# Kernel optimization log

Measured on AMD Instinct MI355X. Metric: run time of the kernel, lower is better.

The kernel has to match this reference:

```python
import jax, jax.numpy as jnp
import numpy as np

RES, K, H = 8192, 48, 128

def _layer_norm(x, g, b, eps=1e-5):
    mu = jnp.mean(x, axis=-1, keepdims=True)
    var = jnp.var(x, axis=-1, keepdims=True)
    return (x - mu) * jax.lax.rsqrt(var + eps) * g + b

def _gelu(x):
    return jax.nn.gelu(x, approximate=False)  # torch default exact GELU

def setup_inputs() -> dict:
    key = jax.random.key(0)
    ks = jax.random.split(key, 16)
    s = 0.05
    inp = {
        "node_h": jax.random.normal(ks[0], (RES, H), jnp.float32),
        "edge_h": jax.random.normal(ks[1], (RES, K, H), jnp.float32),
        "edge_idx": jax.random.randint(ks[2], (RES, K), 0, RES, jnp.int32),
        "seq_emb": jax.random.normal(ks[3], (RES, H), jnp.float32),
        "ar_mask": jax.random.uniform(ks[4], (RES, K), jnp.float32),
        # msg_mlp: Linear(4h,h) -> GELU -> Linear(h,h) -> GELU -> Linear(h,h)
        "mW1": jax.random.normal(ks[5], (4 * H, H), jnp.float32) * s,
        "mb1": jnp.zeros((H,), jnp.float32),
        "mW2": jax.random.normal(ks[6], (H, H), jnp.float32) * s,
        "mb2": jnp.zeros((H,), jnp.float32),
        "mW3": jax.random.normal(ks[7], (H, H), jnp.float32) * s,
        "mb3": jnp.zeros((H,), jnp.float32),
        # ff_node: Linear(h,4h) -> GELU -> Linear(4h,h)
        "fW1": jax.random.normal(ks[8], (H, 4 * H), jnp.float32) * s,
        "fb1": jnp.zeros((4 * H,), jnp.float32),
        "fW2": jax.random.normal(ks[9], (4 * H, H), jnp.float32) * s,
        "fb2": jnp.zeros((H,), jnp.float32),
        "g1": jnp.ones((H,), jnp.float32), "b1": jnp.zeros((H,), jnp.float32),
        "g2": jnp.ones((H,), jnp.float32), "b2": jnp.zeros((H,), jnp.float32),
    }
    return inp

def reference(node_h, edge_h, edge_idx, seq_emb, ar_mask,
              mW1, mb1, mW2, mb2, mW3, mb3,
              fW1, fb1, fW2, fb2, g1, b1, g2, b2):
    seq_j = seq_emb[edge_idx] * ar_mask[..., None]           # [res,k,h]
    e_dec = jnp.concatenate([edge_h, seq_j], axis=-1)        # [res,k,2h]
    h_j = node_h[edge_idx]                                   # [res,k,h]
    h_i = jnp.broadcast_to(node_h[:, None, :], (node_h.shape[0], edge_idx.shape[1], node_h.shape[1]))
    x = jnp.concatenate([h_i, h_j, e_dec], axis=-1)          # [res,k,4h]
    msg = _gelu(x @ mW1 + mb1)
    msg = _gelu(msg @ mW2 + mb2)
    msg = msg @ mW3 + mb3                                    # [res,k,h]
    agg = jnp.sum(msg, axis=1)                               # [res,h]
    h = _layer_norm(node_h + agg, g1, b1)
    ff = _gelu(h @ fW1 + fb1) @ fW2 + fb2
    h = _layer_norm(h + ff, g2, b2)
    return h
```

## Files before the change

### kernel.cpp

```cpp
#include <hip/hip_runtime.h>

#define KNB 48

typedef float  floatx4 __attribute__((ext_vector_type(4)));
typedef __bf16 bf16x8  __attribute__((ext_vector_type(8)));
typedef unsigned short ushort8  __attribute__((ext_vector_type(8)));
typedef unsigned short ushort4v __attribute__((ext_vector_type(4)));

__device__ __forceinline__ float bf2f(unsigned short b) {
  union { unsigned int u; float f; } v; v.u = ((unsigned int)b) << 16; return v.f;
}
__device__ __forceinline__ unsigned short f2bf(float f) {
  __bf16 h = (__bf16)f;
  union { __bf16 h; unsigned short u; } v; v.h = h; return v.u;
}
__device__ __forceinline__ float gelu_f(float x) {
  float u = x * (0.7978845608f + 0.0356774081f * x * x);
  float t = __builtin_amdgcn_exp2f(u * -2.8853900818f);
  return x * __builtin_amdgcn_rcpf(1.0f + t);
}

__global__ __launch_bounds__(256) void k0_transpose(
    const float* mW1, const float* mW2, const float* mW3,
    const float* fW1, const float* fW2,
    unsigned short* MT1, unsigned short* WT2, unsigned short* WT3,
    unsigned short* FWT1, unsigned short* FWT2) {
  __shared__ unsigned short tile[32][33];
  int b = blockIdx.x;
  const float* src; unsigned short* dst; int Kd, Nd, t;
  if (b < 64)       { src = mW1; dst = MT1;  Kd = 512; Nd = 128; t = b; }
  else if (b < 80)  { src = mW2; dst = WT2;  Kd = 128; Nd = 128; t = b - 64; }
  else if (b < 96)  { src = mW3; dst = WT3;  Kd = 128; Nd = 128; t = b - 80; }
  else if (b < 160) { src = fW1; dst = FWT1; Kd = 128; Nd = 512; t = b - 96; }
  else              { src = fW2; dst = FWT2; Kd = 512; Nd = 128; t = b - 160; }
  int tN = Nd >> 5;
  int tk = t / tN, tn = t % tN;
  int tx = threadIdx.x & 31, ty = threadIdx.x >> 5;
  for (int r = 0; r < 4; ++r) {
    int row = ty + r * 8;
    tile[row][tx] = f2bf(src[(size_t)(tk * 32 + row) * Nd + tn * 32 + tx]);
  }
  __syncthreads();
  for (int r = 0; r < 4; ++r) {
    int row = ty + r * 8;
    dst[(size_t)(tn * 32 + row) * Kd + tk * 32 + tx] = tile[tx][row];
  }
}

__global__ __launch_bounds__(256) void k1_nodepre(
    const float* node_h, const float* seq_emb,
    const unsigned short* MT1, const float* mb1,
    float* Apr, unsigned short* BS) {
  __shared__ __align__(16) unsigned short sX[2][32 * 128];
  int r0 = blockIdx.x * 32;
  int tid = threadIdx.x, lane = tid & 63, w = tid >> 6;
  int l15 = lane & 15, l16 = lane >> 4;

  for (int mset = 0; mset < 2; ++mset) {
    const float* src = mset ? (seq_emb + (size_t)r0 * 128) : (node_h + (size_t)r0 * 128);
    for (int k = 0; k < 4; ++k) {
      int f = tid + 256 * k;
      floatx4 v = ((const floatx4*)src)[f];
      int row = f >> 5, hc = f & 31, c = hc >> 1, half = hc & 1;
      ushort4v o;
      o[0] = f2bf(v[0]); o[1] = f2bf(v[1]); o[2] = f2bf(v[2]); o[3] = f2bf(v[3]);
      *(ushort4v*)((char*)&sX[mset][0] + row * 256 + ((c ^ (row & 7)) << 4) + half * 8) = o;
    }
  }
  __syncthreads();

  for (int q = 0; q < 6; ++q) {
    int job = w + 4 * q;
    int kind = job >> 3;
    int nt = job & 7;
    int colOff = (kind == 0) ? 0 : (kind == 1) ? 128 : 384;
    const unsigned short* X = sX[kind == 2 ? 1 : 0];
    bf16x8 wf[4];
    for (int kk = 0; kk < 4; ++kk)
      wf[kk] = *(const bf16x8*)(MT1 + (size_t)(nt * 16 + l15) * 512 + colOff + kk * 32 + l16 * 8);
    for (int mt = 0; mt < 2; ++mt) {
      floatx4 acc = {0.f, 0.f, 0.f, 0.f};
      for (int kk = 0; kk < 4; ++kk) {
        int row = mt * 16 + l15;
        int off = (kk * 64 + l16 * 16) ^ ((row & 7) << 4);
        bf16x8 a = *(const bf16x8*)((const char*)X + row * 256 + off);
        acc = __builtin_amdgcn_mfma_f32_16x16x32_bf16(a, wf[kk], acc, 0, 0, 0);
      }
      int col = nt * 16 + l15;
      for (int r = 0; r < 4; ++r) {
        int row = r0 + mt * 16 + l16 * 4 + r;
        if (kind == 0)      Apr[(size_t)row * 128 + col] = acc[r] + mb1[col];
        else if (kind == 1) BS[(size_t)row * 256 + col] = f2bf(acc[r]);
        else                BS[(size_t)row * 256 + 128 + col] = f2bf(acc[r]);
      }
    }
  }
}

__global__ __launch_bounds__(256) void k2_edge(
    const float* edge_h, const int* edge_idx, const float* ar_mask,
    const unsigned short* MT1, const unsigned short* WT2, const unsigned short* WT3,
    const float* mb2, const float* mb3,
    const float* Apr, const unsigned short* BS,
    float* agg) {
  __shared__ __align__(16) unsigned short sE[96 * 128];
  __shared__ __align__(16) unsigned short sT[96 * 128];
  __shared__ int   sJ[96];
  __shared__ float sM[96];
  int i0 = blockIdx.x * 2;
  int tid = threadIdx.x, lane = tid & 63, w = tid >> 6;
  int l15 = lane & 15, l16 = lane >> 4;
  int rb = (l16 & 1) * 4;

  if (tid < 96) {
    sJ[tid] = edge_idx[(size_t)i0 * KNB + tid];
    sM[tid] = ar_mask[(size_t)i0 * KNB + tid];
  }
  const float* eb = edge_h + (size_t)i0 * KNB * 128;
  for (int k = 0; k < 12; ++k) {
    int f = tid + 256 * k;
    floatx4 v = ((const floatx4*)eb)[f];
    int row = f >> 5, hc = f & 31, c = hc >> 1, half = hc & 1;
    ushort4v o;
    o[0] = f2bf(v[0]); o[1] = f2bf(v[1]); o[2] = f2bf(v[2]); o[3] = f2bf(v[3]);
    *(ushort4v*)((char*)sE + row * 256 + ((c ^ (row & 7)) << 4) + half * 8) = o;
  }
  __syncthreads();

  for (int u = tid; u < 96 * 16; u += 256) {
    int e = u >> 4, c8 = u & 15;
    int j = sJ[e]; float m = sM[e];
    int i = i0 + (e >= 48 ? 1 : 0);
    const floatx4* ap = (const floatx4*)(Apr + (size_t)i * 128 + c8 * 8);
    floatx4 a0 = ap[0], a1 = ap[1];
    ushort8 vb = *(const ushort8*)(BS + (size_t)j * 256 + c8 * 8);
    ushort8 vs = *(const ushort8*)(BS + (size_t)j * 256 + 128 + c8 * 8);
    ushort8 res;
#pragma unroll
    for (int x = 0; x < 4; ++x)
      res[x] = f2bf(a0[x] + bf2f(vb[x]) + m * bf2f(vs[x]));
#pragma unroll
    for (int x = 0; x < 4; ++x)
      res[4 + x] = f2bf(a1[x] + bf2f(vb[4 + x]) + m * bf2f(vs[4 + x]));
    *(ushort8*)((char*)sT + e * 256 + ((c8 ^ (e & 7)) * 16)) = res;
  }
  __syncthreads();

  {
    bf16x8 wf[2][4];
    for (int n = 0; n < 2; ++n)
      for (int kk = 0; kk < 4; ++kk)
        wf[n][kk] = *(const bf16x8*)(MT1 + (size_t)((2 * w + n) * 16 + l15) * 512 + 256 + kk * 32 + l16 * 8);
    int cp0 = ((((2 * w) * 16 + l15) >> 3) << 4) | ((l15 & 7) << 1);
    int cp1 = ((((2 * w + 1) * 16 + l15) >> 3) << 4) | ((l15 & 7) << 1);
    for (int mt = 0; mt < 6; ++mt) {
      floatx4 acc0 = {0.f,0.f,0.f,0.f}, acc1 = {0.f,0.f,0.f,0.f};
      for (int kk = 0; kk < 4; ++kk) {
        int row = mt * 16 + l15;
        int off = (kk * 64 + l16 * 16) ^ ((row & 7) << 4);
        bf16x8 a = *(const bf16x8*)((const char*)sE + row * 256 + off);
        acc0 = __builtin_amdgcn_mfma_f32_16x16x32_bf16(a, wf[0][kk], acc0, 0, 0, 0);
        acc1 = __builtin_amdgcn_mfma_f32_16x16x32_bf16(a, wf[1][kk], acc1, 0, 0, 0);
      }
      char* base = (char*)sT + (mt * 16 + l16 * 4) * 256;
#pragma unroll
      for (int r = 0; r < 4; ++r) {
        int sw = (rb + r) << 4;
        char* p0 = base + r * 256 + (cp0 ^ sw);
        char* p1 = base + r * 256 + (cp1 ^ sw);
        float g0 = bf2f(*(unsigned short*)p0);
        float g1v = bf2f(*(unsigned short*)p1);
        *(unsigned short*)p0 = f2bf(gelu_f(acc0[r] + g0));
        *(unsigned short*)p1 = f2bf(gelu_f(acc1[r] + g1v));
      }
    }
  }
  __syncthreads();

  {
    bf16x8 wf[2][4];
    for (int n = 0; n < 2; ++n)
      for (int kk = 0; kk < 4; ++kk)
        wf[n][kk] = *(const bf16x8*)(WT2 + (size_t)((2 * w + n) * 16 + l15) * 128 + kk * 32 + l16 * 8);
    int cp0 = ((((2 * w) * 16 + l15) >> 3) << 4) | ((l15 & 7) << 1);
    int cp1 = ((((2 * w + 1) * 16 + l15) >> 3) << 4) | ((l15 & 7) << 1);
    float bb0 = mb2[(2 * w) * 16 + l15];
    float bb1 = mb2[(2 * w + 1) * 16 + l15];
    for (int mt = 0; mt < 6; ++mt) {
      floatx4 acc0 = {0.f,0.f,0.f,0.f}, acc1 = {0.f,0.f,0.f,0.f};
      for (int kk = 0; kk < 4; ++kk) {
        int row = mt * 16 + l15;
        int off = (kk * 64 + l16 * 16) ^ ((row & 7) << 4);
        bf16x8 a = *(const bf16x8*)((const char*)sT + row * 256 + off);
        acc0 = __builtin_amdgcn_mfma_f32_16x16x32_bf16(a, wf[0][kk], acc0, 0, 0, 0);
        acc1 = __builtin_amdgcn_mfma_f32_16x16x32_bf16(a, wf[1][kk], acc1, 0, 0, 0);
      }
      char* base = (char*)sE + (mt * 16 + l16 * 4) * 256;
#pragma unroll
      for (int r = 0; r < 4; ++r) {
        int sw = (rb + r) << 4;
        *(unsigned short*)(base + r * 256 + (cp0 ^ sw)) = f2bf(gelu_f(acc0[r] + bb0));
        *(unsigned short*)(base + r * 256 + (cp1 ^ sw)) = f2bf(gelu_f(acc1[r] + bb1));
      }
    }
  }
  __syncthreads();

  {
    bf16x8 wf[2][4];
    for (int n = 0; n < 2; ++n)
      for (int kk = 0; kk < 4; ++kk)
        wf[n][kk] = *(const bf16x8*)(WT3 + (size_t)((2 * w + n) * 16 + l15) * 128 + kk * 32 + l16 * 8);
    for (int half = 0; half < 2; ++half) {
      float agga[2][4] = {{0.f,0.f,0.f,0.f},{0.f,0.f,0.f,0.f}};
      for (int mt3 = 0; mt3 < 3; ++mt3) {
        int mt = half * 3 + mt3;
        floatx4 acc0 = {0.f,0.f,0.f,0.f}, acc1 = {0.f,0.f,0.f,0.f};
        for (int kk = 0; kk < 4; ++kk) {
          int row = mt * 16 + l15;
          int off = (kk * 64 + l16 * 16) ^ ((row & 7) << 4);
          bf16x8 a = *(const bf16x8*)((const char*)sE + row * 256 + off);
          acc0 = __builtin_amdgcn_mfma_f32_16x16x32_bf16(a, wf[0][kk], acc0, 0, 0, 0);
          acc1 = __builtin_amdgcn_mfma_f32_16x16x32_bf16(a, wf[1][kk], acc1, 0, 0, 0);
        }
#pragma unroll
        for (int r = 0; r < 4; ++r) { agga[0][r] += acc0[r]; agga[1][r] += acc1[r]; }
      }
      for (int n = 0; n < 2; ++n) {
        float s = agga[n][0] + agga[n][1] + agga[n][2] + agga[n][3];
        s += __shfl_xor(s, 16);
        s += __shfl_xor(s, 32);
        if (lane < 16) {
          int col = (2 * w + n) * 16 + lane;
          agg[(size_t)(i0 + half) * 128 + col] = s + 48.0f * mb3[col];
        }
      }
    }
  }
}

__global__ __launch_bounds__(256) void k3_ff(
    const float* node_h, const float* agg,
    const unsigned short* FWT1, const unsigned short* FWT2,
    const float* fb1, const float* fb2,
    const float* g1, const float* b1,
    const float* g2, const float* b2,
    float* out) {
  __shared__ __align__(16) unsigned short sH[32 * 128];
  __shared__ __align__(16) unsigned short sT3[32 * 512];
  __shared__ float sP[32 * 128];
  int r0 = blockIdx.x * 32;
  int tid = threadIdx.x, lane = tid & 63, w = tid >> 6;
  int l15 = lane & 15, l16 = lane >> 4;

  {
    int row = tid >> 3;
    int c0 = (tid & 7) * 16;
    const floatx4* nh4 = (const floatx4*)(node_h + (size_t)(r0 + row) * 128 + c0);
    const floatx4* ag4 = (const floatx4*)(agg + (size_t)(r0 + row) * 128 + c0);
    float x[16]; float sum = 0.f, sum2 = 0.f;
#pragma unroll
    for (int q4 = 0; q4 < 4; ++q4) {
      floatx4 a = nh4[q4], g = ag4[q4];
#pragma unroll
      for (int j = 0; j < 4; ++j) {
        float xv = a[j] + g[j];
        x[q4 * 4 + j] = xv; sum += xv; sum2 += xv * xv;
      }
    }
    sum  += __shfl_xor(sum, 1);  sum  += __shfl_xor(sum, 2);  sum  += __shfl_xor(sum, 4);
    sum2 += __shfl_xor(sum2, 1); sum2 += __shfl_xor(sum2, 2); sum2 += __shfl_xor(sum2, 4);
    float mu = sum * (1.f / 128.f);
    float var = sum2 * (1.f / 128.f) - mu * mu;
    float rstd = rsqrtf(var + 1e-5f);
#pragma unroll
    for (int q = 0; q < 16; ++q) {
      int col = c0 + q;
      float h = (x[q] - mu) * rstd * g1[col] + b1[col];
      sP[row * 128 + col] = h;
      char* p = (char*)sH + row * 256 + ((((col >> 3) ^ (row & 7)) << 4) | ((col & 7) << 1));
      *(unsigned short*)p = f2bf(h);
    }
  }
  __syncthreads();

  for (int nq = 0; nq < 8; ++nq) {
    int nt = w * 8 + nq;
    bf16x8 wf[4];
    for (int kk = 0; kk < 4; ++kk)
      wf[kk] = *(const bf16x8*)(FWT1 + (size_t)(nt * 16 + l15) * 128 + kk * 32 + l16 * 8);
    for (int mt = 0; mt < 2; ++mt) {
      floatx4 acc = {0.f,0.f,0.f,0.f};
      for (int kk = 0; kk < 4; ++kk) {
        int row = mt * 16 + l15;
        int off = (kk * 64 + l16 * 16) ^ ((row & 7) << 4);
        bf16x8 a = *(const bf16x8*)((const char*)sH + row * 256 + off);
        acc = __builtin_amdgcn_mfma_f32_16x16x32_bf16(a, wf[kk], acc, 0, 0, 0);
      }
      int col = nt * 16 + l15;
      float bb = fb1[col];
      for (int r = 0; r < 4; ++r) {
        int row = mt * 16 + l16 * 4 + r;
        char* p = (char*)sT3 + row * 1024 + ((((col >> 3) ^ (row & 7)) << 4) | ((col & 7) << 1));
        *(unsigned short*)p = f2bf(gelu_f(acc[r] + bb));
      }
    }
  }
  __syncthreads();

  for (int n = 0; n < 2; ++n) {
    int nt = 2 * w + n;
    for (int mt = 0; mt < 2; ++mt) {
      floatx4 acc = {0.f,0.f,0.f,0.f};
      for (int kk = 0; kk < 16; ++kk) {
        int row = mt * 16 + l15;
        int off = (kk * 64 + l16 * 16) ^ ((row & 7) << 4);
        bf16x8 a = *(const bf16x8*)((const char*)sT3 + row * 1024 + off);
        bf16x8 b = *(const bf16x8*)(FWT2 + (size_t)(nt * 16 + l15) * 512 + kk * 32 + l16 * 8);
        acc = __builtin_amdgcn_mfma_f32_16x16x32_bf16(a, b, acc, 0, 0, 0);
      }
      int col = nt * 16 + l15;
      float bb = fb2[col];
      for (int r = 0; r < 4; ++r) {
        int row = mt * 16 + l16 * 4 + r;
        sP[row * 128 + col] += acc[r] + bb;
      }
    }
  }
  __syncthreads();

  {
    int row = tid >> 3;
    int c0 = (tid & 7) * 16;
    float x[16]; float sum = 0.f, sum2 = 0.f;
#pragma unroll
    for (int q = 0; q < 16; ++q) {
      float xv = sP[row * 128 + c0 + q];
      x[q] = xv; sum += xv; sum2 += xv * xv;
    }
    sum  += __shfl_xor(sum, 1);  sum  += __shfl_xor(sum, 2);  sum  += __shfl_xor(sum, 4);
    sum2 += __shfl_xor(sum2, 1); sum2 += __shfl_xor(sum2, 2); sum2 += __shfl_xor(sum2, 4);
    float mu = sum * (1.f / 128.f);
    float var = sum2 * (1.f / 128.f) - mu * mu;
    float rstd = rsqrtf(var + 1e-5f);
#pragma unroll
    for (int q = 0; q < 16; ++q) {
      int col = c0 + q;
      out[(size_t)(r0 + row) * 128 + col] = (x[q] - mu) * rstd * g2[col] + b2[col];
    }
  }
}

extern "C" void kernel_launch(void* const* d_in, const int* in_sizes, int n_in,
                              void* d_out, int out_size, void* d_ws, size_t ws_size,
                              hipStream_t stream) {
  const float* node_h  = (const float*)d_in[0];
  const float* edge_h  = (const float*)d_in[1];
  const int*   edge_idx= (const int*)d_in[2];
  const float* seq_emb = (const float*)d_in[3];
  const float* ar_mask = (const float*)d_in[4];
  const float* mW1 = (const float*)d_in[5];
  const float* mb1 = (const float*)d_in[6];
  const float* mW2 = (const float*)d_in[7];
  const float* mb2 = (const float*)d_in[8];
  const float* mW3 = (const float*)d_in[9];
  const float* mb3 = (const float*)d_in[10];
  const float* fW1 = (const float*)d_in[11];
  const float* fb1 = (const float*)d_in[12];
  const float* fW2 = (const float*)d_in[13];
  const float* fb2 = (const float*)d_in[14];
  const float* g1  = (const float*)d_in[15];
  const float* b1  = (const float*)d_in[16];
  const float* g2  = (const float*)d_in[17];
  const float* b2  = (const float*)d_in[18];

  char* ws = (char*)d_ws;
  unsigned short* MT1  = (unsigned short*)(ws + 0);
  unsigned short* WT2  = (unsigned short*)(ws + 131072);
  unsigned short* WT3  = (unsigned short*)(ws + 163840);
  unsigned short* FWT1 = (unsigned short*)(ws + 196608);
  unsigned short* FWT2 = (unsigned short*)(ws + 327680);
  float*          Apr  = (float*)(ws + 458752);
  unsigned short* BS   = (unsigned short*)(ws + 4653056);
  float*          agg  = (float*)(ws + 8847360);

  hipLaunchKernelGGL(k0_transpose, dim3(224), dim3(256), 0, stream,
                     mW1, mW2, mW3, fW1, fW2, MT1, WT2, WT3, FWT1, FWT2);
  hipLaunchKernelGGL(k1_nodepre, dim3(256), dim3(256), 0, stream,
                     node_h, seq_emb, MT1, mb1, Apr, BS);
  hipLaunchKernelGGL(k2_edge, dim3(4096), dim3(256), 0, stream,
                     edge_h, edge_idx, ar_mask, MT1, WT2, WT3, mb2, mb3,
                     Apr, BS, agg);
  hipLaunchKernelGGL(k3_ff, dim3(256), dim3(256), 0, stream,
                     node_h, agg, FWT1, FWT2, fb1, fb2, g1, b1, g2, b2,
                     (float*)d_out);
}
```

Before: 144.1 us.

## Double k2_edge block to 512 threads, one output column tile per wave

```diff
diff --git a/kernel.cpp b/kernel.cpp
--- a/kernel.cpp
+++ b/kernel.cpp
@@ -97,7 +97,7 @@
   }
 }
 
-__global__ __launch_bounds__(256) void k2_edge(
+__global__ __launch_bounds__(512) void k2_edge(
     const float* edge_h, const int* edge_idx, const float* ar_mask,
     const unsigned short* MT1, const unsigned short* WT2, const unsigned short* WT3,
     const float* mb2, const float* mb3,
@@ -105,31 +105,29 @@
     float* agg) {
   __shared__ __align__(16) unsigned short sE[96 * 128];
   __shared__ __align__(16) unsigned short sT[96 * 128];
-  __shared__ int   sJ[96];
-  __shared__ float sM[96];
   int i0 = blockIdx.x * 2;
   int tid = threadIdx.x, lane = tid & 63, w = tid >> 6;
   int l15 = lane & 15, l16 = lane >> 4;
   int rb = (l16 & 1) * 4;
-
-  if (tid < 96) {
-    sJ[tid] = edge_idx[(size_t)i0 * KNB + tid];
-    sM[tid] = ar_mask[(size_t)i0 * KNB + tid];
-  }
+  int colw = w * 16 + l15;
+  int cp = ((colw >> 3) << 4) | ((l15 & 7) << 1);
+
   const float* eb = edge_h + (size_t)i0 * KNB * 128;
-  for (int k = 0; k < 12; ++k) {
-    int f = tid + 256 * k;
+#pragma unroll
+  for (int k = 0; k < 6; ++k) {
+    int f = tid + 512 * k;
     floatx4 v = ((const floatx4*)eb)[f];
     int row = f >> 5, hc = f & 31, c = hc >> 1, half = hc & 1;
     ushort4v o;
     o[0] = f2bf(v[0]); o[1] = f2bf(v[1]); o[2] = f2bf(v[2]); o[3] = f2bf(v[3]);
     *(ushort4v*)((char*)sE + row * 256 + ((c ^ (row & 7)) << 4) + half * 8) = o;
   }
-  __syncthreads();
-
-  for (int u = tid; u < 96 * 16; u += 256) {
+#pragma unroll
+  for (int k = 0; k < 3; ++k) {
+    int u = tid + 512 * k;
     int e = u >> 4, c8 = u & 15;
-    int j = sJ[e]; float m = sM[e];
+    int j = edge_idx[(size_t)i0 * KNB + e];
+    float m = ar_mask[(size_t)i0 * KNB + e];
     int i = i0 + (e >= 48 ? 1 : 0);
     const floatx4* ap = (const floatx4*)(Apr + (size_t)i * 128 + c8 * 8);
     floatx4 a0 = ap[0], a1 = ap[1];
@@ -147,93 +145,82 @@
   __syncthreads();
 
   {
-    bf16x8 wf[2][4];
-    for (int n = 0; n < 2; ++n)
-      for (int kk = 0; kk < 4; ++kk)
-        wf[n][kk] = *(const bf16x8*)(MT1 + (size_t)((2 * w + n) * 16 + l15) * 512 + 256 + kk * 32 + l16 * 8);
-    int cp0 = ((((2 * w) * 16 + l15) >> 3) << 4) | ((l15 & 7) << 1);
-    int cp1 = ((((2 * w + 1) * 16 + l15) >> 3) << 4) | ((l15 & 7) << 1);
+    bf16x8 wf[4];
+#pragma unroll
+    for (int kk = 0; kk < 4; ++kk)
+      wf[kk] = *(const bf16x8*)(MT1 + (size_t)colw * 512 + 256 + kk * 32 + l16 * 8);
     for (int mt = 0; mt < 6; ++mt) {
-      floatx4 acc0 = {0.f,0.f,0.f,0.f}, acc1 = {0.f,0.f,0.f,0.f};
+      floatx4 acc = {0.f,0.f,0.f,0.f};
+#pragma unroll
       for (int kk = 0; kk < 4; ++kk) {
         int row = mt * 16 + l15;
         int off = (kk * 64 + l16 * 16) ^ ((row & 7) << 4);
         bf16x8 a = *(const bf16x8*)((const char*)sE + row * 256 + off);
-        acc0 = __builtin_amdgcn_mfma_f32_16x16x32_bf16(a, wf[0][kk], acc0, 0, 0, 0);
-        acc1 = __builtin_amdgcn_mfma_f32_16x16x32_bf16(a, wf[1][kk], acc1, 0, 0, 0);
+        acc = __builtin_amdgcn_mfma_f32_16x16x32_bf16(a, wf[kk], acc, 0, 0, 0);
       }
       char* base = (char*)sT + (mt * 16 + l16 * 4) * 256;
 #pragma unroll
       for (int r = 0; r < 4; ++r) {
-        int sw = (rb + r) << 4;
-        char* p0 = base + r * 256 + (cp0 ^ sw);
-        char* p1 = base + r * 256 + (cp1 ^ sw);
-        float g0 = bf2f(*(unsigned short*)p0);
-        float g1v = bf2f(*(unsigned short*)p1);
-        *(unsigned short*)p0 = f2bf(gelu_f(acc0[r] + g0));
-        *(unsigned short*)p1 = f2bf(gelu_f(acc1[r] + g1v));
-      }
-    }
-  }
-  __syncthreads();
-
-  {
-    bf16x8 wf[2][4];
-    for (int n = 0; n < 2; ++n)
-      for (int kk = 0; kk < 4; ++kk)
-        wf[n][kk] = *(const bf16x8*)(WT2 + (size_t)((2 * w + n) * 16 + l15) * 128 + kk * 32 + l16 * 8);
-    int cp0 = ((((2 * w) * 16 + l15) >> 3) << 4) | ((l15 & 7) << 1);
-    int cp1 = ((((2 * w + 1) * 16 + l15) >> 3) << 4) | ((l15 & 7) << 1);
-    float bb0 = mb2[(2 * w) * 16 + l15];
-    float bb1 = mb2[(2 * w + 1) * 16 + l15];
+        char* p = base + r * 256 + (cp ^ ((rb + r) << 4));
+        float g = bf2f(*(unsigned short*)p);
+        *(unsigned short*)p = f2bf(gelu_f(acc[r] + g));
+      }
+    }
+  }
+  __syncthreads();
+
+  {
+    bf16x8 wf[4];
+#pragma unroll
+    for (int kk = 0; kk < 4; ++kk)
+      wf[kk] = *(const bf16x8*)(WT2 + (size_t)colw * 128 + kk * 32 + l16 * 8);
+    float bb = mb2[colw];
     for (int mt = 0; mt < 6; ++mt) {
-      floatx4 acc0 = {0.f,0.f,0.f,0.f}, acc1 = {0.f,0.f,0.f,0.f};
+      floatx4 acc = {0.f,0.f,0.f,0.f};
+#pragma unroll
       for (int kk = 0; kk < 4; ++kk) {
         int row = mt * 16 + l15;
         int off = (kk * 64 + l16 * 16) ^ ((row & 7) << 4);
         bf16x8 a = *(const bf16x8*)((const char*)sT + row * 256 + off);
-        acc0 = __builtin_amdgcn_mfma_f32_16x16x32_bf16(a, wf[0][kk], acc0, 0, 0, 0);
-        acc1 = __builtin_amdgcn_mfma_f32_16x16x32_bf16(a, wf[1][kk], acc1, 0, 0, 0);
+        acc = __builtin_amdgcn_mfma_f32_16x16x32_bf16(a, wf[kk], acc, 0, 0, 0);
       }
       char* base = (char*)sE + (mt * 16 + l16 * 4) * 256;
 #pragma unroll
       for (int r = 0; r < 4; ++r) {
-        int sw = (rb + r) << 4;
-        *(unsigned short*)(base + r * 256 + (cp0 ^ sw)) = f2bf(gelu_f(acc0[r] + bb0));
-        *(unsigned short*)(base + r * 256 + (cp1 ^ sw)) = f2bf(gelu_f(acc1[r] + bb1));
-      }
-    }
-  }
-  __syncthreads();
-
-  {
-    bf16x8 wf[2][4];
-    for (int n = 0; n < 2; ++n)
-      for (int kk = 0; kk < 4; ++kk)
-        wf[n][kk] = *(const bf16x8*)(WT3 + (size_t)((2 * w + n) * 16 + l15) * 128 + kk * 32 + l16 * 8);
+        char* p = base + r * 256 + (cp ^ ((rb + r) << 4));
+        *(unsigned short*)p = f2bf(gelu_f(acc[r] + bb));
+      }
+    }
+  }
+  __syncthreads();
+
+  {
+    bf16x8 wf[4];
+#pragma unroll
+    for (int kk = 0; kk < 4; ++kk)
+      wf[kk] = *(const bf16x8*)(WT3 + (size_t)colw * 128 + kk * 32 + l16 * 8);
+#pragma unroll
     for (int half = 0; half < 2; ++half) {
-      float agga[2][4] = {{0.f,0.f,0.f,0.f},{0.f,0.f,0.f,0.f}};
+      float agga[4] = {0.f,0.f,0.f,0.f};
       for (int mt3 = 0; mt3 < 3; ++mt3) {
         int mt = half * 3 + mt3;
-        floatx4 acc0 = {0.f,0.f,0.f,0.f}, acc1 = {0.f,0.f,0.f,0.f};
+        floatx4 acc = {0.f,0.f,0.f,0.f};
+#pragma unroll
         for (int kk = 0; kk < 4; ++kk) {
           int row = mt * 16 + l15;
           int off = (kk * 64 + l16 * 16) ^ ((row & 7) << 4);
           bf16x8 a = *(const bf16x8*)((const char*)sE + row * 256 + off);
-          acc0 = __builtin_amdgcn_mfma_f32_16x16x32_bf16(a, wf[0][kk], acc0, 0, 0, 0);
-          acc1 = __builtin_amdgcn_mfma_f32_16x16x32_bf16(a, wf[1][kk], acc1, 0, 0, 0);
+          acc = __builtin_amdgcn_mfma_f32_16x16x32_bf16(a, wf[kk], acc, 0, 0, 0);
         }
 #pragma unroll
-        for (int r = 0; r < 4; ++r) { agga[0][r] += acc0[r]; agga[1][r] += acc1[r]; }
-      }
-      for (int n = 0; n < 2; ++n) {
-        float s = agga[n][0] + agga[n][1] + agga[n][2] + agga[n][3];
-        s += __shfl_xor(s, 16);
-        s += __shfl_xor(s, 32);
-        if (lane < 16) {
-          int col = (2 * w + n) * 16 + lane;
-          agg[(size_t)(i0 + half) * 128 + col] = s + 48.0f * mb3[col];
-        }
+        for (int r = 0; r < 4; ++r) agga[r] += acc[r];
+      }
+      float s = agga[0] + agga[1] + agga[2] + agga[3];
+      s += __shfl_xor(s, 16);
+      s += __shfl_xor(s, 32);
+      if (lane < 16) {
+        int col = w * 16 + lane;
+        agg[(size_t)(i0 + half) * 128 + col] = s + 48.0f * mb3[col];
       }
     }
   }
@@ -388,7 +375,7 @@
                      mW1, mW2, mW3, fW1, fW2, MT1, WT2, WT3, FWT1, FWT2);
   hipLaunchKernelGGL(k1_nodepre, dim3(256), dim3(256), 0, stream,
                      node_h, seq_emb, MT1, mb1, Apr, BS);
-  hipLaunchKernelGGL(k2_edge, dim3(4096), dim3(256), 0, stream,
+  hipLaunchKernelGGL(k2_edge, dim3(4096), dim3(512), 0, stream,
                      edge_h, edge_idx, ar_mask, MT1, WT2, WT3, mb2, mb3,
                      Apr, BS, agg);
   hipLaunchKernelGGL(k3_ff, dim3(256), dim3(256), 0, stream,
```

Measured after the change: 139.5 us. 3.1% less time.
